# Performance work log

Hardware: AMD Instinct MI355X
Metric: run time of the kernel (lower is better)

The kernel has to match this reference:

```python
import jax, jax.numpy as jnp
import numpy as np

NUM_HEADS = 16
HEAD_DIM = 128
D = NUM_HEADS * HEAD_DIM  # 2048
B, S = 4, 2048
NEG = jnp.finfo(jnp.float32).min


def setup_inputs() -> dict:
    key = jax.random.key(0)
    ks = jax.random.split(key, 6)
    scale = 1.0 / np.sqrt(D)
    return {
        "hidden_states": jax.random.normal(ks[0], (B, S, D), jnp.float32),
        "wq": jax.random.normal(ks[1], (D, D), jnp.float32) * scale,
        "wk": jax.random.normal(ks[2], (D, D), jnp.float32) * scale,
        "wv": jax.random.normal(ks[3], (D, D), jnp.float32) * scale,
        "wo": jax.random.normal(ks[4], (D, D), jnp.float32) * scale,
        "bo": jnp.zeros((D,), jnp.float32),
    }


def _split_heads(x):
    b, s, _ = x.shape
    return x.reshape(b, s, NUM_HEADS, HEAD_DIM).transpose(0, 2, 1, 3)  # [B,H,S,Dh]


def reference(hidden_states, wq, wk, wv, wo, bo):
    # projections (nn.Linear: x @ W^T), no bias for q/k/v
    q = _split_heads(hidden_states @ wq.T).astype(jnp.float32)
    k = _split_heads(hidden_states @ wk.T).astype(jnp.float32)
    v = _split_heads(hidden_states @ wv.T)
    # GPT-Neo: NO 1/sqrt(d) scaling
    scores = jnp.einsum("bhqd,bhkd->bhqk", q, k)  # [B,H,S,S] fp32
    s = scores.shape[-1]
    causal = jnp.tril(jnp.ones((s, s), bool))  # [S,S]
    scores = jnp.where(causal[None, None], scores, NEG)
    attn_weights = jax.nn.softmax(scores, axis=-1).astype(v.dtype)
    # dropout is identity at eval (p=0.0)
    attn_output = jnp.einsum("bhqk,bhkd->bhqd", attn_weights, v)
    attn_output = attn_output.transpose(0, 2, 1, 3).reshape(hidden_states.shape)
    attn_output = attn_output @ wo.T + bo
    return attn_output, attn_weights
```

## Files before the change

kernel.cpp:

```cpp
#include <hip/hip_runtime.h>

#define DEVFN static __device__ __forceinline__

typedef _Float16 f16;
typedef f16 f16x8 __attribute__((ext_vector_type(8)));
typedef f16 f16x4 __attribute__((ext_vector_type(4)));
typedef float f32x4 __attribute__((ext_vector_type(4)));
typedef short short8 __attribute__((ext_vector_type(8)));

constexpr int Bc = 4, Hn = 16, Sn = 2048, DH = 128, Dn = 2048;
constexpr long MROWS = (long)Bc * Sn;
constexpr long LDQK = 2 * Dn;

template <typename T, typename C>
DEVFN auto mfma_impl(T a, T b, C c, int)
    -> decltype(__builtin_amdgcn_mfma_f32_16x16x32_f16(a, b, c, 0, 0, 0)) {
  return __builtin_amdgcn_mfma_f32_16x16x32_f16(a, b, c, 0, 0, 0);
}
template <typename T, typename C>
DEVFN C mfma_impl(T a, T b, C c, long) {
  return __builtin_amdgcn_mfma_f32_16x16x32_f16(
      __builtin_bit_cast(short8, a), __builtin_bit_cast(short8, b), c, 0, 0, 0);
}
DEVFN f32x4 MFMA(f16x8 a, f16x8 b, f32x4 c) { return mfma_impl(a, b, c, 0); }

DEVFN void nt_store(float* p, float v) { __builtin_nontemporal_store(v, p); }
DEVFN void nt_store4(float* p, f32x4 v) {
  __builtin_nontemporal_store(v, (f32x4*)p);
}

DEVFN void gld_lds16(const f16* g, f16* s) {
  __builtin_amdgcn_global_load_lds(
      (const __attribute__((address_space(1))) unsigned int*)g,
      (__attribute__((address_space(3))) unsigned int*)s, 16, 0, 0);
}

DEVFN void stage_tile(const f16* __restrict__ g, long ld, f16* __restrict__ s) {
  const int t = threadIdx.x;
  const int rr = t >> 3;
  const int cb = (t & 7) * 16;
#pragma unroll
  for (int ch = 0; ch < 4; ++ch) {
    const int r = ch * 32 + rr;
    const int scb = cb ^ ((r & 7) << 4);
    gld_lds16(g + (long)r * ld + (scb >> 1), s + r * 64 + (cb >> 1));
  }
}

DEVFN void stage_tile128(const f16* __restrict__ g, long ld, f16* __restrict__ s) {
  const int t = threadIdx.x;
  const int rr = t >> 4;
  const int cb = (t & 15) * 16;
#pragma unroll
  for (int ch = 0; ch < 8; ++ch) {
    const int r = ch * 16 + rr;
    const int scb = cb ^ ((r & 7) << 4);
    gld_lds16(g + (long)r * ld + (scb >> 1), s + r * 128 + (cb >> 1));
  }
}

DEVFN f16x8 ldfrag(const f16* s, int row, int kelem) {
  const int cb = (kelem * 2) ^ ((row & 7) << 4);
  return *(const f16x8*)(s + row * 64 + (cb >> 1));
}

DEVFN f16x8 ldfrag128(const f16* s, int row, int kelem) {
  const int cb = (kelem * 2) ^ ((row & 7) << 4);
  return *(const f16x8*)((const char*)s + row * 256 + cb);
}

DEVFN f16x8 ldfrag64(const f16* s, int row, int kelem) {
  const int cb = (kelem * 2) ^ ((row & 7) << 4);
  return *(const f16x8*)((const char*)s + row * 128 + cb);
}

__global__ __launch_bounds__(256) void k_cvt_all(
    const float* __restrict__ hid, const float* __restrict__ wq,
    const float* __restrict__ wk, const float* __restrict__ wv,
    const float* __restrict__ wo, f16* __restrict__ h16,
    f16* __restrict__ wqk16, f16* __restrict__ wv16, f16* __restrict__ wo16) {
  const int y = blockIdx.y;
  const long nW = (long)Dn * Dn;
  const float* x;
  f16* out;
  if (y < 4) {
    x = hid + (long)y * nW;
    out = h16 + (long)y * nW;
  } else if (y == 4) {
    x = wq; out = wqk16;
  } else if (y == 5) {
    x = wk; out = wqk16 + nW;
  } else if (y == 6) {
    x = wv; out = wv16;
  } else {
    x = wo; out = wo16;
  }
  const long i = ((long)blockIdx.x * 256 + threadIdx.x) * 4;
  float4 v = *(const float4*)(x + i);
  f16x4 h;
  h[0] = (f16)v.x; h[1] = (f16)v.y; h[2] = (f16)v.z; h[3] = (f16)v.w;
  *(f16x4*)(out + i) = h;
}

DEVFN void gemm_body(const f16* __restrict__ A, long ldA,
                     const f16* __restrict__ B, long ldB, int K,
                     f16* __restrict__ oh, long ldC, int nt, int mt,
                     float oscale, f16* sA, f16* sB) {
  const int tid = threadIdx.x, w = tid >> 6, lane = tid & 63;
  const int wm = (w >> 1) * 64, wn = (w & 1) * 64;
  const int lr = lane & 15, lg = lane >> 4;
  f32x4 acc[4][4] = {};
  const f16* Ab = A + (long)mt * 128 * ldA;
  const f16* Bb = B + (long)nt * 128 * ldB;

  stage_tile(Ab, ldA, sA);
  stage_tile(Bb, ldB, sB);
  __syncthreads();

  int cur = 0;
  for (int kt = 0; kt < K; kt += 64) {
    if (kt + 64 < K) {
      stage_tile(Ab + kt + 64, ldA, sA + (cur ^ 1) * (128 * 64));
      stage_tile(Bb + kt + 64, ldB, sB + (cur ^ 1) * (128 * 64));
    }
    const f16* cA = sA + cur * (128 * 64);
    const f16* cB = sB + cur * (128 * 64);
#pragma unroll
    for (int kk = 0; kk < 64; kk += 32) {
      f16x8 ahf[4], bhf[4];
#pragma unroll
      for (int m = 0; m < 4; ++m) ahf[m] = ldfrag(cA, wm + m * 16 + lr, kk + lg * 8);
#pragma unroll
      for (int n = 0; n < 4; ++n) bhf[n] = ldfrag(cB, wn + n * 16 + lr, kk + lg * 8);
#pragma unroll
      for (int m = 0; m < 4; ++m)
#pragma unroll
        for (int n = 0; n < 4; ++n) acc[m][n] = MFMA(ahf[m], bhf[n], acc[m][n]);
    }
    __syncthreads();
    cur ^= 1;
  }

#pragma unroll
  for (int m = 0; m < 4; ++m)
#pragma unroll
    for (int n = 0; n < 4; ++n) {
      const int col = nt * 128 + wn + n * 16 + lr;
#pragma unroll
      for (int r = 0; r < 4; ++r) {
        const long row = (long)mt * 128 + wm + m * 16 + lg * 4 + r;
        oh[row * ldC + col] = (f16)(acc[m][n][r] * oscale);
      }
    }
}

__global__ __launch_bounds__(256) void k_fused(
    const f16* __restrict__ h16, const f16* __restrict__ wqk16,
    const f16* __restrict__ wv16, f16* __restrict__ qk16, f16* __restrict__ vT,
    float* __restrict__ wts) {
  __shared__ __align__(16) f16 sA[2 * 128 * 64];
  __shared__ __align__(16) f16 sB[2 * 128 * 64];
  const int bid = blockIdx.x;
  if ((bid & 3) == 3) {
    const int zid = bid >> 2;
    const int bh = zid & 63, qt = zid >> 6;
    const int ncols = Sn - (qt + 1) * 128;
    if (ncols <= 0) return;
    float* base = wts + (long)bh * Sn * Sn + (long)qt * 128 * Sn + (qt + 1) * 128;
    const int tid = threadIdx.x;
    const f32x4 z = {0.f, 0.f, 0.f, 0.f};
    for (int r = 0; r < 128; ++r) {
      float* rowp = base + (long)r * Sn;
      for (int c = tid * 4; c < ncols; c += 1024) nt_store4(rowp + c, z);
    }
    return;
  }
  const int gid = 3 * (bid >> 2) + (bid & 3);
  if (gid < 2048) {
    const int cpx = 2048 >> 3;
    const int swz = (gid & 7) * cpx + (gid >> 3);
    const int nt = swz & 31, mt = swz >> 5;
    const float qsc = (nt < 16) ? 1.44269504f : 1.0f;
    gemm_body(h16, Dn, wqk16, Dn, Dn, qk16, LDQK, nt, mt, qsc, sA, sB);
  } else {
    const int sb = gid - 2048;
    const int cpx = 1024 >> 3;
    const int swz = (sb & 7) * cpx + (sb >> 3);
    const int nt = swz & 63, mt = swz >> 6;
    gemm_body(wv16, Dn, h16, Dn, Dn, vT, MROWS, nt, mt, 1.0f, sA, sB);
  }
}

__global__ __launch_bounds__(256) void k_gemm_wo(
    const f16* __restrict__ A, const f16* __restrict__ B,
    float* __restrict__ of, const float* __restrict__ bias) {
  const int nwgx = gridDim.x;
  const int nwg = nwgx * gridDim.y;
  const int bid = blockIdx.y * nwgx + blockIdx.x;
  const int cpx = nwg >> 3;
  const int swz = (bid & 7) * cpx + (bid >> 3);
  const int nt = swz % nwgx, mt = swz / nwgx;
  __shared__ __align__(16) f16 sA[2][128 * 64];
  __shared__ __align__(16) f16 sB[2][128 * 64];
  const int tid = threadIdx.x, w = tid >> 6, lane = tid & 63;
  const int wm = (w >> 1) * 64, wn = (w & 1) * 64;
  const int lr = lane & 15, lg = lane >> 4;
  f32x4 acc[4][4] = {};
  const f16* Ab = A + (long)mt * 128 * Dn;
  const f16* Bb = B + (long)nt * 128 * Dn;

  stage_tile(Ab, Dn, sA[0]);
  stage_tile(Bb, Dn, sB[0]);
  __syncthreads();

  int cur = 0;
  for (int kt = 0; kt < Dn; kt += 64) {
    if (kt + 64 < Dn) {
      stage_tile(Ab + kt + 64, Dn, sA[cur ^ 1]);
      stage_tile(Bb + kt + 64, Dn, sB[cur ^ 1]);
    }
#pragma unroll
    for (int kk = 0; kk < 64; kk += 32) {
      f16x8 ahf[4], bhf[4];
#pragma unroll
      for (int m = 0; m < 4; ++m) ahf[m] = ldfrag(sA[cur], wm + m * 16 + lr, kk + lg * 8);
#pragma unroll
      for (int n = 0; n < 4; ++n) bhf[n] = ldfrag(sB[cur], wn + n * 16 + lr, kk + lg * 8);
#pragma unroll
      for (int m = 0; m < 4; ++m)
#pragma unroll
        for (int n = 0; n < 4; ++n) acc[m][n] = MFMA(ahf[m], bhf[n], acc[m][n]);
    }
    __syncthreads();
    cur ^= 1;
  }

#pragma unroll
  for (int m = 0; m < 4; ++m)
#pragma unroll
    for (int n = 0; n < 4; ++n) {
      const int col = nt * 128 + wn + n * 16 + lr;
#pragma unroll
      for (int r = 0; r < 4; ++r) {
        const long row = (long)mt * 128 + wm + m * 16 + lg * 4 + r;
        nt_store(of + row * Dn + col, acc[m][n][r] + bias[col]);
      }
    }
}

__global__ __launch_bounds__(256) void k_attn(const f16* __restrict__ qk16,
                                              const f16* __restrict__ vT,
                                              float* __restrict__ wts,
                                              f16* __restrict__ ctx) {
  const int wgid = blockIdx.x;
  const int xcd = wgid & 7, slot = wgid >> 3;
  const int bh = xcd + 8 * (slot >> 4);
  const int qt = 15 - (slot & 15);
  const int b = bh >> 4, h = bh & 15;
  const int tid = threadIdx.x, wv = tid >> 6, lane = tid & 63;
  const int lr = lane & 15, lg = lane >> 4;
  const f16* Qb = qk16 + ((long)b * Sn + qt * 128) * LDQK + h * DH;
  const f16* Kb = qk16 + (long)b * Sn * LDQK + Dn + h * DH;
  const f16* Vb = vT + (long)h * DH * MROWS + (long)b * Sn;
  float* Wrow = wts + (long)bh * Sn * Sn + (long)qt * 128 * Sn;
  __shared__ __align__(16) f16 sK[2][128 * 128];
  __shared__ __align__(16) f16 sQW[128 * 64];

  const int krr = tid >> 4;
  const int kce = (tid & 15) * 8;
  const int kcb = kce * 2;
  f16x8 kpf[8];

#define PRE_K(kt_)                                                              \
  {                                                                             \
    const long kbase = (long)(kt_)*128;                                         \
    _Pragma("unroll") for (int ch = 0; ch < 8; ++ch) kpf[ch] =                  \
        *(const f16x8*)(Kb + (kbase + ch * 16 + krr) * LDQK + kce);             \
  }
#define PUB_K(buf)                                                              \
  {                                                                             \
    _Pragma("unroll") for (int ch = 0; ch < 8; ++ch) {                          \
      const int r = ch * 16 + krr;                                              \
      *(f16x8*)((char*)(buf) + r * 256 + (kcb ^ ((r & 7) << 4))) = kpf[ch];     \
    }                                                                           \
  }

  stage_tile128(Qb, LDQK, sK[0]);
  PRE_K(0);
  __syncthreads();
  const int wq0 = wv * 32;
  f16x8 qf[2][4];
#pragma unroll
  for (int m = 0; m < 2; ++m)
#pragma unroll
    for (int kk = 0; kk < 4; ++kk)
      qf[m][kk] = ldfrag128(sK[0], wq0 + m * 16 + lr, kk * 32 + lg * 8);
  __syncthreads();
  PUB_K(sK[0]);
  if (qt > 0) PRE_K(1);
  __syncthreads();
  int cur = 0;

  float rs[2][4] = {};
  for (int kt = 0; kt <= qt; ++kt) {
    f32x4 acc[2][8] = {};
#pragma unroll
    for (int kk = 0; kk < 4; ++kk) {
      f16x8 bf[8];
#pragma unroll
      for (int n = 0; n < 8; ++n) bf[n] = ldfrag128(sK[cur], n * 16 + lr, kk * 32 + lg * 8);
#pragma unroll
      for (int m = 0; m < 2; ++m)
#pragma unroll
        for (int n = 0; n < 8; ++n) acc[m][n] = MFMA(qf[m][kk], bf[n], acc[m][n]);
    }
    if (kt + 1 <= qt) PUB_K(sK[cur ^ 1]);
    PRE_K(kt + 2 <= qt ? kt + 2 : 0);
    const bool diag = (kt == qt);
#pragma unroll
    for (int m = 0; m < 2; ++m)
#pragma unroll
      for (int r = 0; r < 4; ++r) {
        const int row = wq0 + m * 16 + lg * 4 + r;
        float ts = 0.f;
#pragma unroll
        for (int n = 0; n < 8; ++n) {
          const bool ok = !diag || (n * 16 + lr) <= row;
          ts += ok ? __builtin_amdgcn_exp2f(acc[m][n][r]) : 0.f;
        }
        rs[m][r] += ts;
      }
    __syncthreads();
    cur ^= 1;
  }
  float ri[2][4];
#pragma unroll
  for (int m = 0; m < 2; ++m)
#pragma unroll
    for (int r = 0; r < 4; ++r) {
      float s = rs[m][r];
#pragma unroll
      for (int o = 1; o < 16; o <<= 1) s += __shfl_xor(s, o, 64);
      ri[m][r] = 1.f / s;
    }

  PUB_K(sK[cur ^ 1]);
  if (qt > 0) PRE_K(1);
  __syncthreads();
  cur ^= 1;

  const int ro = lane >> 3, cg = lane & 7;
  f32x4 pacc[2][8] = {};
  for (int kt = 0; kt <= qt; ++kt) {
    f32x4 sacc[2][8] = {};
#pragma unroll
    for (int kk = 0; kk < 4; ++kk) {
      f16x8 bf[8];
#pragma unroll
      for (int n = 0; n < 8; ++n) bf[n] = ldfrag128(sK[cur], n * 16 + lr, kk * 32 + lg * 8);
#pragma unroll
      for (int m = 0; m < 2; ++m)
#pragma unroll
        for (int n = 0; n < 8; ++n) sacc[m][n] = MFMA(qf[m][kk], bf[n], sacc[m][n]);
    }
    if (kt + 1 <= qt) PUB_K(sK[cur ^ 1]);
    if (kt + 2 <= qt) PRE_K(kt + 2);
    const bool diag = (kt == qt);
#pragma unroll
    for (int hf = 0; hf < 2; ++hf) {
#pragma unroll
      for (int m = 0; m < 2; ++m)
#pragma unroll
        for (int n = hf * 4; n < hf * 4 + 4; ++n) {
          const int col = n * 16 + lr;
          const int scol = col - hf * 64;
#pragma unroll
          for (int r = 0; r < 4; ++r) {
            const int row = wq0 + m * 16 + lg * 4 + r;
            float w = __builtin_amdgcn_exp2f(sacc[m][n][r]) * ri[m][r];
            if (diag && col > row) w = 0.f;
            *(f16*)((char*)sQW + row * 128 + ((scol * 2) ^ ((row & 7) << 4))) = (f16)w;
          }
        }
#pragma unroll
      for (int it = 0; it < 4; ++it) {
        const int row = wq0 + it * 8 + ro;
        f16x8 v = ldfrag64(sQW, row, cg * 8);
        f32x4 lo = {(float)v[0], (float)v[1], (float)v[2], (float)v[3]};
        f32x4 hi = {(float)v[4], (float)v[5], (float)v[6], (float)v[7]};
        float* wp = Wrow + (long)row * Sn + kt * 128 + hf * 64 + cg * 8;
        nt_store4(wp, lo);
        nt_store4(wp + 4, hi);
      }
#pragma unroll
      for (int kk = 0; kk < 2; ++kk) {
        f16x8 af[2], bfr[8];
#pragma unroll
        for (int m = 0; m < 2; ++m)
          af[m] = ldfrag64(sQW, wq0 + m * 16 + lr, kk * 32 + lg * 8);
#pragma unroll
        for (int n = 0; n < 8; ++n)
          bfr[n] = *(const f16x8*)(Vb + (long)(n * 16 + lr) * MROWS + kt * 128 + hf * 64 + kk * 32 + lg * 8);
#pragma unroll
        for (int m = 0; m < 2; ++m)
#pragma unroll
          for (int n = 0; n < 8; ++n) pacc[m][n] = MFMA(af[m], bfr[n], pacc[m][n]);
      }
    }
    __syncthreads();
    cur ^= 1;
  }

#pragma unroll
  for (int m = 0; m < 2; ++m)
#pragma unroll
    for (int n = 0; n < 8; ++n) {
      const int d = n * 16 + lr;
#pragma unroll
      for (int r = 0; r < 4; ++r) {
        const int q = qt * 128 + wq0 + m * 16 + lg * 4 + r;
        ctx[(long)(b * Sn + q) * Dn + h * DH + d] = (f16)pacc[m][n][r];
      }
    }
#undef PRE_K
#undef PUB_K
}

extern "C" void kernel_launch(void* const* d_in, const int* in_sizes, int n_in,
                              void* d_out, int out_size, void* d_ws, size_t ws_size,
                              hipStream_t stream) {
  const float* hid = (const float*)d_in[0];
  const float* wq = (const float*)d_in[1];
  const float* wk = (const float*)d_in[2];
  const float* wv = (const float*)d_in[3];
  const float* wo = (const float*)d_in[4];
  const float* bo = (const float*)d_in[5];
  float* out = (float*)d_out;
  float* wts = out + (long)Bc * Sn * Dn;

  char* ws = (char*)d_ws;
  const long MB = 1 << 20;
  f16* h16 = (f16*)(ws + 0 * MB);
  f16* wqk16 = (f16*)(ws + 32 * MB);
  f16* wv16 = (f16*)(ws + 48 * MB);
  f16* wo16 = (f16*)(ws + 56 * MB);
  f16* qk16 = (f16*)(ws + 64 * MB);
  f16* vT = (f16*)(ws + 128 * MB);
  f16* ctx = (f16*)(ws + 160 * MB);

  k_cvt_all<<<dim3(4096, 8), 256, 0, stream>>>(
      hid, wq, wk, wv, wo, h16, wqk16, wv16, wo16);
  k_fused<<<4096, 256, 0, stream>>>(h16, wqk16, wv16, qk16, vT, wts);
  k_attn<<<1024, 256, 0, stream>>>(qk16, vT, wts, ctx);
  k_gemm_wo<<<dim3(16, 64), 256, 0, stream>>>(ctx, wo16, out, bo);
}
```

Before: 805.8 us.

## Drop LDS staging of attention weights; reload previous tile from global for PV

Attention weights are now written straight from MFMA accumulators to global memory with scalar fp32 stores, replacing the LDS-transposed vectorized non-temporal stores. The PV product for each tile is deferred by one iteration and reads the weights back from global memory (likely L2-resident), converting them to fp16. This removes the sQW LDS buffer and its round trips, which may raise occupancy. In exchange the stores become strided and uncoalesced, and every weight tile is read back from memory.

```diff
diff --git a/kernel.cpp b/kernel.cpp
--- a/kernel.cpp
+++ b/kernel.cpp
@@ -67,11 +67,6 @@
 DEVFN f16x8 ldfrag128(const f16* s, int row, int kelem) {
   const int cb = (kelem * 2) ^ ((row & 7) << 4);
   return *(const f16x8*)((const char*)s + row * 256 + cb);
-}
-
-DEVFN f16x8 ldfrag64(const f16* s, int row, int kelem) {
-  const int cb = (kelem * 2) ^ ((row & 7) << 4);
-  return *(const f16x8*)((const char*)s + row * 128 + cb);
 }
 
 __global__ __launch_bounds__(256) void k_cvt_all(
@@ -264,7 +259,6 @@
   const f16* Vb = vT + (long)h * DH * MROWS + (long)b * Sn;
   float* Wrow = wts + (long)bh * Sn * Sn + (long)qt * 128 * Sn;
   __shared__ __align__(16) f16 sK[2][128 * 128];
-  __shared__ __align__(16) f16 sQW[128 * 64];
 
   const int krr = tid >> 4;
   const int kce = (tid & 15) * 8;
@@ -282,6 +276,28 @@
     _Pragma("unroll") for (int ch = 0; ch < 8; ++ch) {                          \
       const int r = ch * 16 + krr;                                              \
       *(f16x8*)((char*)(buf) + r * 256 + (kcb ^ ((r & 7) << 4))) = kpf[ch];     \
+    }                                                                           \
+  }
+#define PV_TILE(j)                                                              \
+  {                                                                             \
+    _Pragma("unroll") for (int kk = 0; kk < 4; ++kk) {                          \
+      f16x8 af[2], bfr[8];                                                      \
+      _Pragma("unroll") for (int m = 0; m < 2; ++m) {                           \
+        const float* wp =                                                       \
+            Wrow + (long)(wq0 + m * 16 + lr) * Sn + (j)*128 + kk * 32 + lg * 8; \
+        float4 x0 = *(const float4*)wp;                                         \
+        float4 x1 = *(const float4*)(wp + 4);                                   \
+        f16x8 t;                                                                \
+        t[0] = (f16)x0.x; t[1] = (f16)x0.y; t[2] = (f16)x0.z; t[3] = (f16)x0.w; \
+        t[4] = (f16)x1.x; t[5] = (f16)x1.y; t[6] = (f16)x1.z; t[7] = (f16)x1.w; \
+        af[m] = t;                                                              \
+      }                                                                         \
+      _Pragma("unroll") for (int n = 0; n < 8; ++n) bfr[n] =                    \
+          *(const f16x8*)(Vb + (long)(n * 16 + lr) * MROWS + (j)*128 +          \
+                          kk * 32 + lg * 8);                                    \
+      _Pragma("unroll") for (int m = 0; m < 2; ++m)                             \
+          _Pragma("unroll") for (int n = 0; n < 8; ++n) pacc[m][n] =            \
+          MFMA(af[m], bfr[n], pacc[m][n]);                                      \
     }                                                                           \
   }
 
@@ -349,7 +365,6 @@
   __syncthreads();
   cur ^= 1;
 
-  const int ro = lane >> 3, cg = lane & 7;
   f32x4 pacc[2][8] = {};
   for (int kt = 0; kt <= qt; ++kt) {
     f32x4 sacc[2][8] = {};
@@ -367,49 +382,23 @@
     if (kt + 2 <= qt) PRE_K(kt + 2);
     const bool diag = (kt == qt);
 #pragma unroll
-    for (int hf = 0; hf < 2; ++hf) {
-#pragma unroll
-      for (int m = 0; m < 2; ++m)
-#pragma unroll
-        for (int n = hf * 4; n < hf * 4 + 4; ++n) {
-          const int col = n * 16 + lr;
-          const int scol = col - hf * 64;
-#pragma unroll
-          for (int r = 0; r < 4; ++r) {
-            const int row = wq0 + m * 16 + lg * 4 + r;
-            float w = __builtin_amdgcn_exp2f(sacc[m][n][r]) * ri[m][r];
-            if (diag && col > row) w = 0.f;
-            *(f16*)((char*)sQW + row * 128 + ((scol * 2) ^ ((row & 7) << 4))) = (f16)w;
-          }
+    for (int m = 0; m < 2; ++m)
+#pragma unroll
+      for (int n = 0; n < 8; ++n) {
+        const int col = n * 16 + lr;
+#pragma unroll
+        for (int r = 0; r < 4; ++r) {
+          const int row = wq0 + m * 16 + lg * 4 + r;
+          float w = __builtin_amdgcn_exp2f(sacc[m][n][r]) * ri[m][r];
+          if (diag && col > row) w = 0.f;
+          Wrow[(long)row * Sn + kt * 128 + col] = w;
         }
-#pragma unroll
-      for (int it = 0; it < 4; ++it) {
-        const int row = wq0 + it * 8 + ro;
-        f16x8 v = ldfrag64(sQW, row, cg * 8);
-        f32x4 lo = {(float)v[0], (float)v[1], (float)v[2], (float)v[3]};
-        f32x4 hi = {(float)v[4], (float)v[5], (float)v[6], (float)v[7]};
-        float* wp = Wrow + (long)row * Sn + kt * 128 + hf * 64 + cg * 8;
-        nt_store4(wp, lo);
-        nt_store4(wp + 4, hi);
       }
-#pragma unroll
-      for (int kk = 0; kk < 2; ++kk) {
-        f16x8 af[2], bfr[8];
-#pragma unroll
-        for (int m = 0; m < 2; ++m)
-          af[m] = ldfrag64(sQW, wq0 + m * 16 + lr, kk * 32 + lg * 8);
-#pragma unroll
-        for (int n = 0; n < 8; ++n)
-          bfr[n] = *(const f16x8*)(Vb + (long)(n * 16 + lr) * MROWS + kt * 128 + hf * 64 + kk * 32 + lg * 8);
-#pragma unroll
-        for (int m = 0; m < 2; ++m)
-#pragma unroll
-          for (int n = 0; n < 8; ++n) pacc[m][n] = MFMA(af[m], bfr[n], pacc[m][n]);
-      }
-    }
+    if (kt > 0) PV_TILE(kt - 1);
     __syncthreads();
     cur ^= 1;
   }
+  PV_TILE(qt);
 
 #pragma unroll
   for (int m = 0; m < 2; ++m)
@@ -424,6 +413,7 @@
     }
 #undef PRE_K
 #undef PUB_K
+#undef PV_TILE
 }
 
 extern "C" void kernel_launch(void* const* d_in, const int* in_sizes, int n_in,
```

Measured after the change: 1.077 ms (median of 2 runs). 1.34x slower.
